# Kernel tuning notes

Hardware: AMD Instinct MI355X
Metric: run time of the kernel (lower is better)

## Reference

```python
import jax, jax.numpy as jnp
import numpy as np

B, N, K, H = 4, 2048, 48, 128
EDGE = 128
FF = 4 * H
SCALE = 30.0


def setup_inputs() -> dict:
    key = jax.random.key(0)
    ks = jax.random.split(key, 12)
    s = lambda fan_in: 1.0 / np.sqrt(fan_in)
    return {
        "h_V": jax.random.normal(ks[0], (B, N, H), jnp.float32),
        "h_E": jax.random.normal(ks[1], (B, N, K, EDGE), jnp.float32),
        "E_idx": jax.random.randint(ks[2], (B, N, K), 0, N, jnp.int32),
        "mask_V": jnp.ones((B, N), jnp.float32),
        "mask_attend": jnp.ones((B, N, K), jnp.float32),
        "W1_w": jax.random.normal(ks[3], (H + EDGE, H), jnp.float32) * s(H + EDGE),
        "W1_b": jnp.zeros((H,), jnp.float32),
        "W2_w": jax.random.normal(ks[4], (H, H), jnp.float32) * s(H),
        "W2_b": jnp.zeros((H,), jnp.float32),
        "W3_w": jax.random.normal(ks[5], (H, H), jnp.float32) * s(H),
        "W3_b": jnp.zeros((H,), jnp.float32),
        "Win_w": jax.random.normal(ks[6], (H, FF), jnp.float32) * s(H),
        "Win_b": jnp.zeros((FF,), jnp.float32),
        "Wout_w": jax.random.normal(ks[7], (FF, H), jnp.float32) * s(FF),
        "Wout_b": jnp.zeros((H,), jnp.float32),
    }


def reference(h_V, h_E, E_idx, mask_V, mask_attend,
              W1_w, W1_b, W2_w, W2_b, W3_w, W3_b,
              Win_w, Win_b, Wout_w, Wout_b):
    gelu_tanh = lambda x: jax.nn.gelu(x, approximate=True)   # self.act = jax.nn.gelu (default approx)
    gelu_exact = lambda x: jax.nn.gelu(x, approximate=False)  # FFN uses approximate=False

    # gather neighbor node features: [B,N,K,H]
    h_nb = jax.vmap(lambda hv, idx: hv[idx])(h_V, E_idx)
    h_EV = jnp.concatenate([h_nb, h_E], axis=-1)              # [B,N,K,H+EDGE]

    # 3-layer message MLP
    m = gelu_tanh(jnp.einsum('bnkc,ch->bnkh', h_EV, W1_w) + W1_b)
    m = gelu_tanh(jnp.einsum('bnkh,hg->bnkg', m, W2_w) + W2_b)
    m = jnp.einsum('bnkg,gh->bnkh', m, W3_w) + W3_b

    m = mask_attend[..., None] * m
    dh = jnp.sum(m, axis=-2) / SCALE                          # [B,N,H]
    h = h_V + dh                                              # dropout rate 0 (eval)

    # position-wise FFN
    ff = gelu_exact(jnp.einsum('bnh,hf->bnf', h, Win_w) + Win_b)
    dh2 = jnp.einsum('bnf,fh->bnh', ff, Wout_w) + Wout_b
    h = h + dh2

    return mask_V[..., None] * h
```

## Files before the change

### kernel.cpp

```cpp
#include <hip/hip_runtime.h>
#include <hip/hip_bf16.h>
#include <math.h>

typedef __attribute__((ext_vector_type(8))) short bf16x8;
typedef __attribute__((ext_vector_type(4))) float f32x4;

#define MFMA16(a,b,c) __builtin_amdgcn_mfma_f32_16x16x32_bf16((a),(b),(c),0,0,0)

__device__ __forceinline__ unsigned int pack2(float a, float b){
  __hip_bfloat162 h = __float22bfloat162_rn(float2{a, b});
  union { __hip_bfloat162 h; unsigned int u; } v; v.h = h;
  return v.u;
}
__device__ __forceinline__ float gelu_tanh_f(float x){
  float x2 = x * x;
  float z  = x * fmaf(x2, -0.10294823f, -2.3022082f);
  float e  = exp2f(z);
  return x * __builtin_amdgcn_rcpf(1.0f + e);
}
__device__ __forceinline__ float gelu_erf_f(float x){
  return 0.5f * x * (1.0f + erff(x * 0.70710678118654752f));
}

__global__ void k_prep(const float* __restrict__ W1, const float* __restrict__ W2,
                       const float* __restrict__ W3, const float* __restrict__ Win,
                       const float* __restrict__ Wout, unsigned short* __restrict__ wt)
{
  int t = blockIdx.x * 256 + threadIdx.x;
  if (t >= 196608) return;
  float v;
  if (t < 32768){            int o = t >> 8,        i = t & 255;         v = W1[i*128 + o]; }
  else if (t < 49152){       int l = t - 32768, o = l >> 7, i = l & 127; v = W2[i*128 + o]; }
  else if (t < 65536){       int l = t - 49152, o = l >> 7, i = l & 127; v = W3[i*128 + o]; }
  else if (t < 131072){      int l = t - 65536, o = l >> 7, i = l & 127; v = Win[i*512 + o]; }
  else {                     int l = t - 131072, o = l >> 9, i = l & 511; v = Wout[i*128 + o]; }
  union { float f; unsigned int u; } w; w.f = v;
  unsigned int r = w.u + 0x7fffu + ((w.u >> 16) & 1u);
  wt[t] = (unsigned short)(r >> 16);
}

__global__ __launch_bounds__(256)
void k_hvp(const float* __restrict__ hV, const unsigned short* __restrict__ wt,
           const float* __restrict__ b1, float* __restrict__ hVp)
{
  __shared__ char sH[32*256];
  const int tid = threadIdx.x;
  const int wv  = tid >> 6;
  const int ln  = tid & 63;
  const int l15 = ln & 15;
  const int l4  = ln >> 4;
  const int swz = (l15 & 7) << 4;
  const unsigned short* W1T = wt;
  const int nb = blockIdx.x * 32;

#pragma unroll
  for (int it = 0; it < 2; ++it){
    int cid = tid + it*256;
    int r = cid >> 4, cb = cid & 15;
    const float* src = hV + (size_t)(nb + r)*128 + cb*8;
    float4 a0 = *(const float4*)(src);
    float4 a1 = *(const float4*)(src + 4);
    uint4 w;
    w.x = pack2(a0.x, a0.y); w.y = pack2(a0.z, a0.w);
    w.z = pack2(a1.x, a1.y); w.w = pack2(a1.z, a1.w);
    *(uint4*)(&sH[r*256 + ((cb*16) ^ ((r&7)<<4))]) = w;
  }
  __syncthreads();

  f32x4 acc[2][2];
#pragma unroll
  for (int m = 0; m < 2; ++m){ acc[m][0] = f32x4{0.f,0.f,0.f,0.f}; acc[m][1] = f32x4{0.f,0.f,0.f,0.f}; }
#pragma unroll
  for (int ks = 0; ks < 4; ++ks){
    bf16x8 x0 = *(const bf16x8*)(&sH[(l15)*256      + ((ks*64 + l4*16) ^ swz)]);
    bf16x8 x1 = *(const bf16x8*)(&sH[(16 + l15)*256 + ((ks*64 + l4*16) ^ swz)]);
#pragma unroll
    for (int m = 0; m < 2; ++m){
      int orow = (wv*2 + m)*16 + l15;
      bf16x8 wf = *(const bf16x8*)(W1T + orow*256 + ks*32 + l4*8);
      acc[m][0] = MFMA16(wf, x0, acc[m][0]);
      acc[m][1] = MFMA16(wf, x1, acc[m][1]);
    }
  }
#pragma unroll
  for (int m = 0; m < 2; ++m){
    int och0 = (wv*2 + m)*16 + l4*4;
    float q0 = b1[och0], q1 = b1[och0+1], q2 = b1[och0+2], q3 = b1[och0+3];
#pragma unroll
    for (int nt = 0; nt < 2; ++nt){
      int node = nb + nt*16 + l15;
      float4 o;
      o.x = acc[m][nt][0] + q0;
      o.y = acc[m][nt][1] + q1;
      o.z = acc[m][nt][2] + q2;
      o.w = acc[m][nt][3] + q3;
      *(float4*)(hVp + (size_t)node*128 + och0) = o;
    }
  }
}

#define NPB 4
__global__ __launch_bounds__(512, 4)
void k_msg(const float* __restrict__ hE, const int* __restrict__ Eidx,
           const float* __restrict__ maskA, const unsigned short* __restrict__ wt,
           const float* __restrict__ hVp, const float* __restrict__ b2,
           float* __restrict__ S, float* __restrict__ msums)
{
  __shared__ char sE0[12288];
  __shared__ char sE1[12288];
  __shared__ char sM [12288];

  const int tid = threadIdx.x;
  const int wv  = tid >> 6;
  const int ln  = tid & 63;
  const int l15 = ln & 15;
  const int l4  = ln >> 4;
  const int swz = (l15 & 7) << 4;

  const unsigned short* W1T = wt;
  const unsigned short* W2T = wt + 32768;

  bf16x8 w1f[4], w2f[4];
  {
    int orow = wv*16 + l15;
#pragma unroll
    for (int ks = 0; ks < 4; ++ks){
      w1f[ks] = *(const bf16x8*)(W1T + orow*256 + 128 + ks*32 + l4*8);
      w2f[ks] = *(const bf16x8*)(W2T + orow*128 + ks*32 + l4*8);
    }
  }
  const int och0 = wv*16 + l4*4;
  const float4 b2q = *(const float4*)(b2 + och0);

  int xoff[4];
#pragma unroll
  for (int ks = 0; ks < 4; ++ks) xoff[ks] = l15*256 + ((ks*64 + l4*16) ^ swz);
  const int woff  = l15*256 + ((och0*2) ^ swz);
  const int soff0 = (tid>>5)*256 + (((tid&31)*8) ^ (((tid>>5)&7)<<4));

  const int node0 = blockIdx.x * NPB;

  float4 e0, e1, e2;
  int pidx0, pidx1, pidx2; float pmk0, pmk1, pmk2;
  {
    const float4* ef = (const float4*)(hE + (size_t)node0 * 6144);
    e0 = ef[tid]; e1 = ef[tid + 512]; e2 = ef[tid + 1024];
    const int* ip = Eidx + node0*48 + l15;
    pidx0 = ip[0]; pidx1 = ip[16]; pidx2 = ip[32];
    const float* mp = maskA + node0*48 + l15;
    pmk0 = mp[0]; pmk1 = mp[16]; pmk2 = mp[32];
  }

  auto body = [&](char* sE, int node){
    const int b = node >> 11;
    const float mk0 = pmk0, mk1 = pmk1, mk2 = pmk2;
    float4 hp0, hp1, hp2;
    {
      const float* base = hVp + ((size_t)(b << 11)) * 128 + och0;
      hp0 = *(const float4*)(base + (size_t)pidx0 * 128);
      hp1 = *(const float4*)(base + (size_t)pidx1 * 128);
      hp2 = *(const float4*)(base + (size_t)pidx2 * 128);
    }
    {
      uint2 p;
      p.x = pack2(e0.x, e0.y); p.y = pack2(e0.z, e0.w);
      *(uint2*)(sE + soff0) = p;
      p.x = pack2(e1.x, e1.y); p.y = pack2(e1.z, e1.w);
      *(uint2*)(sE + soff0 + 4096) = p;
      p.x = pack2(e2.x, e2.y); p.y = pack2(e2.z, e2.w);
      *(uint2*)(sE + soff0 + 8192) = p;
    }
    {
      int pn = (node + 1 < 8192) ? node + 1 : node;
      const float4* ef = (const float4*)(hE + (size_t)pn * 6144);
      e0 = ef[tid]; e1 = ef[tid + 512]; e2 = ef[tid + 1024];
      const int* ip = Eidx + pn*48 + l15;
      pidx0 = ip[0]; pidx1 = ip[16]; pidx2 = ip[32];
      const float* mp = maskA + pn*48 + l15;
      pmk0 = mp[0]; pmk1 = mp[16]; pmk2 = mp[32];
    }
    __syncthreads();

    f32x4 a0 = f32x4{0.f,0.f,0.f,0.f}, a1 = a0, a2 = a0;
#pragma unroll
    for (int ks = 0; ks < 4; ++ks){
      bf16x8 x0 = *(const bf16x8*)(sE + xoff[ks]);
      bf16x8 x1 = *(const bf16x8*)(sE + xoff[ks] + 4096);
      bf16x8 x2 = *(const bf16x8*)(sE + xoff[ks] + 8192);
      a0 = MFMA16(w1f[ks], x0, a0);
      a1 = MFMA16(w1f[ks], x1, a1);
      a2 = MFMA16(w1f[ks], x2, a2);
    }
    {
      uint2 p;
      p.x = pack2(gelu_tanh_f(a0[0] + hp0.x), gelu_tanh_f(a0[1] + hp0.y));
      p.y = pack2(gelu_tanh_f(a0[2] + hp0.z), gelu_tanh_f(a0[3] + hp0.w));
      *(uint2*)(sM + woff) = p;
      p.x = pack2(gelu_tanh_f(a1[0] + hp1.x), gelu_tanh_f(a1[1] + hp1.y));
      p.y = pack2(gelu_tanh_f(a1[2] + hp1.z), gelu_tanh_f(a1[3] + hp1.w));
      *(uint2*)(sM + woff + 4096) = p;
      p.x = pack2(gelu_tanh_f(a2[0] + hp2.x), gelu_tanh_f(a2[1] + hp2.y));
      p.y = pack2(gelu_tanh_f(a2[2] + hp2.z), gelu_tanh_f(a2[3] + hp2.w));
      *(uint2*)(sM + woff + 8192) = p;
    }
    __syncthreads();

    a0 = f32x4{0.f,0.f,0.f,0.f}; a1 = a0; a2 = a0;
#pragma unroll
    for (int ks = 0; ks < 4; ++ks){
      bf16x8 x0 = *(const bf16x8*)(sM + xoff[ks]);
      bf16x8 x1 = *(const bf16x8*)(sM + xoff[ks] + 4096);
      bf16x8 x2 = *(const bf16x8*)(sM + xoff[ks] + 8192);
      a0 = MFMA16(w2f[ks], x0, a0);
      a1 = MFMA16(w2f[ks], x1, a1);
      a2 = MFMA16(w2f[ks], x2, a2);
    }
    {
      float s0, s1, s2, s3;
      s0  = mk0 * gelu_tanh_f(a0[0] + b2q.x);
      s1  = mk0 * gelu_tanh_f(a0[1] + b2q.y);
      s2  = mk0 * gelu_tanh_f(a0[2] + b2q.z);
      s3  = mk0 * gelu_tanh_f(a0[3] + b2q.w);
      s0 += mk1 * gelu_tanh_f(a1[0] + b2q.x);
      s1 += mk1 * gelu_tanh_f(a1[1] + b2q.y);
      s2 += mk1 * gelu_tanh_f(a1[2] + b2q.z);
      s3 += mk1 * gelu_tanh_f(a1[3] + b2q.w);
      s0 += mk2 * gelu_tanh_f(a2[0] + b2q.x);
      s1 += mk2 * gelu_tanh_f(a2[1] + b2q.y);
      s2 += mk2 * gelu_tanh_f(a2[2] + b2q.z);
      s3 += mk2 * gelu_tanh_f(a2[3] + b2q.w);
#pragma unroll
      for (int off = 1; off < 16; off <<= 1){
        s0 += __shfl_xor(s0, off, 16);
        s1 += __shfl_xor(s1, off, 16);
        s2 += __shfl_xor(s2, off, 16);
        s3 += __shfl_xor(s3, off, 16);
      }
      if (l15 == 0){
        float4 o;
        o.x = s0 * (1.0f/30.0f);
        o.y = s1 * (1.0f/30.0f);
        o.z = s2 * (1.0f/30.0f);
        o.w = s3 * (1.0f/30.0f);
        *(float4*)(S + (size_t)node*128 + och0) = o;
      }
      if (wv == 0){
        float q = mk0 + mk1 + mk2;
#pragma unroll
        for (int off = 1; off < 16; off <<= 1) q += __shfl_xor(q, off, 16);
        if (ln == 0) msums[node] = q * (1.0f/30.0f);
      }
    }
  };

#pragma unroll
  for (int i = 0; i < NPB; i += 2){
    body(sE0, node0 + i);
    body(sE1, node0 + i + 1);
  }
}

__global__ __launch_bounds__(256, 2)
void k_ffn(const float* __restrict__ hV, const float* __restrict__ S,
           const float* __restrict__ msums, const float* __restrict__ maskV,
           const unsigned short* __restrict__ wt,
           const float* __restrict__ b3, const float* __restrict__ bin,
           const float* __restrict__ bout, float* __restrict__ out)
{
  __shared__ char  sS[32*256];
  __shared__ char  sH[32*256];
  __shared__ float sHf[32*132];
  __shared__ char  sF[32*1024];

  const int tid = threadIdx.x;
  const int wv  = tid >> 6;
  const int ln  = tid & 63;
  const int l15 = ln & 15;
  const int l4  = ln >> 4;
  const int swz = (l15 & 7) << 4;
  const unsigned short* W3T   = wt + 49152;
  const unsigned short* WinT  = wt + 65536;
  const unsigned short* WoutT = wt + 131072;
  const int nb = blockIdx.x * 32;

#pragma unroll
  for (int it = 0; it < 2; ++it){
    int cid = tid + it*256;
    int r = cid >> 4, cb = cid & 15;
    const float* src = S + (size_t)(nb + r)*128 + cb*8;
    float4 a0 = *(const float4*)(src);
    float4 a1 = *(const float4*)(src + 4);
    uint4 w;
    w.x = pack2(a0.x, a0.y); w.y = pack2(a0.z, a0.w);
    w.z = pack2(a1.x, a1.y); w.w = pack2(a1.z, a1.w);
    *(uint4*)(&sS[r*256 + ((cb*16) ^ ((r&7)<<4))]) = w;
  }
  __syncthreads();

  {
    f32x4 acc[2][2];
#pragma unroll
    for (int m = 0; m < 2; ++m){ acc[m][0] = f32x4{0.f,0.f,0.f,0.f}; acc[m][1] = f32x4{0.f,0.f,0.f,0.f}; }
#pragma unroll
    for (int ks = 0; ks < 4; ++ks){
      bf16x8 x0 = *(const bf16x8*)(&sS[(l15)*256      + ((ks*64 + l4*16) ^ swz)]);
      bf16x8 x1 = *(const bf16x8*)(&sS[(16 + l15)*256 + ((ks*64 + l4*16) ^ swz)]);
#pragma unroll
      for (int m = 0; m < 2; ++m){
        int cr = (wv*2 + m)*16 + l15;
        bf16x8 wf = *(const bf16x8*)(W3T + cr*128 + ks*32 + l4*8);
        acc[m][0] = MFMA16(wf, x0, acc[m][0]);
        acc[m][1] = MFMA16(wf, x1, acc[m][1]);
      }
    }
#pragma unroll
    for (int m = 0; m < 2; ++m){
      int ch0 = (wv*2 + m)*16 + l4*4;
      const float4 b3q = *(const float4*)(b3 + ch0);
#pragma unroll
      for (int nt = 0; nt < 2; ++nt){
        int row  = nt*16 + l15;
        int node = nb + row;
        float ms = msums[node];
        const float4 hv = *(const float4*)(hV + (size_t)node*128 + ch0);
        float h0 = hv.x + acc[m][nt][0] + ms*b3q.x;
        float h1 = hv.y + acc[m][nt][1] + ms*b3q.y;
        float h2 = hv.z + acc[m][nt][2] + ms*b3q.z;
        float h3 = hv.w + acc[m][nt][3] + ms*b3q.w;
        float4 hf; hf.x = h0; hf.y = h1; hf.z = h2; hf.w = h3;
        *(float4*)(&sHf[row*132 + ch0]) = hf;
        uint2 p; p.x = pack2(h0, h1); p.y = pack2(h2, h3);
        *(uint2*)(&sH[row*256 + ((ch0*2) ^ ((row&7)<<4))]) = p;
      }
    }
  }
  __syncthreads();

  f32x4 accA[8][2];
#pragma unroll
  for (int m8 = 0; m8 < 8; ++m8){ accA[m8][0] = f32x4{0.f,0.f,0.f,0.f}; accA[m8][1] = f32x4{0.f,0.f,0.f,0.f}; }
#pragma unroll
  for (int ks = 0; ks < 4; ++ks){
    bf16x8 x0 = *(const bf16x8*)(&sH[(l15)*256      + ((ks*64 + l4*16) ^ swz)]);
    bf16x8 x1 = *(const bf16x8*)(&sH[(16 + l15)*256 + ((ks*64 + l4*16) ^ swz)]);
#pragma unroll
    for (int m8 = 0; m8 < 8; ++m8){
      int fr = (wv*8 + m8)*16 + l15;
      bf16x8 wf = *(const bf16x8*)(WinT + fr*128 + ks*32 + l4*8);
      accA[m8][0] = MFMA16(wf, x0, accA[m8][0]);
      accA[m8][1] = MFMA16(wf, x1, accA[m8][1]);
    }
  }
#pragma unroll
  for (int m8 = 0; m8 < 8; ++m8){
    int f0 = (wv*8 + m8)*16 + l4*4;
    float q0 = bin[f0], q1 = bin[f0+1], q2 = bin[f0+2], q3 = bin[f0+3];
#pragma unroll
    for (int nt = 0; nt < 2; ++nt){
      int row = nt*16 + l15;
      float g0 = gelu_erf_f(accA[m8][nt][0] + q0);
      float g1 = gelu_erf_f(accA[m8][nt][1] + q1);
      float g2 = gelu_erf_f(accA[m8][nt][2] + q2);
      float g3 = gelu_erf_f(accA[m8][nt][3] + q3);
      uint2 p; p.x = pack2(g0, g1); p.y = pack2(g2, g3);
      *(uint2*)(&sF[row*1024 + ((f0*2) ^ swz)]) = p;
    }
  }
  __syncthreads();

  f32x4 accB[2][2];
#pragma unroll
  for (int m = 0; m < 2; ++m){ accB[m][0] = f32x4{0.f,0.f,0.f,0.f}; accB[m][1] = f32x4{0.f,0.f,0.f,0.f}; }
#pragma unroll
  for (int ks = 0; ks < 16; ++ks){
    bf16x8 x0 = *(const bf16x8*)(&sF[(l15)*1024      + ((ks*64 + l4*16) ^ swz)]);
    bf16x8 x1 = *(const bf16x8*)(&sF[(16 + l15)*1024 + ((ks*64 + l4*16) ^ swz)]);
#pragma unroll
    for (int m = 0; m < 2; ++m){
      int cr = (wv*2 + m)*16 + l15;
      bf16x8 wf = *(const bf16x8*)(WoutT + cr*512 + ks*32 + l4*8);
      accB[m][0] = MFMA16(wf, x0, accB[m][0]);
      accB[m][1] = MFMA16(wf, x1, accB[m][1]);
    }
  }
#pragma unroll
  for (int m = 0; m < 2; ++m){
    int ch0 = (wv*2 + m)*16 + l4*4;
    float q0 = bout[ch0], q1 = bout[ch0+1], q2 = bout[ch0+2], q3 = bout[ch0+3];
#pragma unroll
    for (int nt = 0; nt < 2; ++nt){
      int row  = nt*16 + l15;
      int node = nb + row;
      float mv = maskV[node];
      const float4 hf = *(const float4*)(&sHf[row*132 + ch0]);
      float4 o;
      o.x = mv * (hf.x + accB[m][nt][0] + q0);
      o.y = mv * (hf.y + accB[m][nt][1] + q1);
      o.z = mv * (hf.z + accB[m][nt][2] + q2);
      o.w = mv * (hf.w + accB[m][nt][3] + q3);
      *(float4*)(out + (size_t)node*128 + ch0) = o;
    }
  }
}

extern "C" void kernel_launch(void* const* d_in, const int* in_sizes, int n_in,
                              void* d_out, int out_size, void* d_ws, size_t ws_size,
                              hipStream_t stream)
{
  const float* hV    = (const float*)d_in[0];
  const float* hE    = (const float*)d_in[1];
  const int*   Eidx  = (const int*)  d_in[2];
  const float* maskV = (const float*)d_in[3];
  const float* maskA = (const float*)d_in[4];
  const float* W1w = (const float*)d_in[5];
  const float* W1b = (const float*)d_in[6];
  const float* W2w = (const float*)d_in[7];
  const float* W2b = (const float*)d_in[8];
  const float* W3w = (const float*)d_in[9];
  const float* W3b = (const float*)d_in[10];
  const float* Winw  = (const float*)d_in[11];
  const float* Winb  = (const float*)d_in[12];
  const float* Woutw = (const float*)d_in[13];
  const float* Woutb = (const float*)d_in[14];
  float* out = (float*)d_out;

  unsigned short* wt = (unsigned short*)d_ws;
  float* hVp   = (float*)((char*)d_ws + (1u << 19));
  float* Sbuf  = (float*)((char*)d_ws + (1u << 19) + (1u << 22));
  float* msums = (float*)((char*)d_ws + (1u << 19) + (2u << 22));

  k_prep<<<dim3(768),  dim3(256), 0, stream>>>(W1w, W2w, W3w, Winw, Woutw, wt);
  k_hvp <<<dim3(256),  dim3(256), 0, stream>>>(hV, wt, W1b, hVp);
  k_msg <<<dim3(2048), dim3(512), 0, stream>>>(hE, Eidx, maskA, wt, hVp, W2b, Sbuf, msums);
  k_ffn <<<dim3(256),  dim3(256), 0, stream>>>(hV, Sbuf, msums, maskV, wt, W3b, Winb, Woutb, out);
}
```

Baseline: 117.5 us.

## Retile message kernel to two nodes per step and store gathered projections in bf16

The message kernel now handles two nodes per iteration, with two groups of four waves. Each wave computes 32 output channels over 48 edges, so each LDS operand read feeds two MFMAs, and the sE/sM buffers are merged into one double-buffered 24KB buffer. The weight fragments are reloaded from global memory each tile instead of being held in registers, which cuts register pressure but adds L2 traffic. The precomputed h_V projection is stored as bf16, halving the bytes of the random neighbour gather at some precision cost. The grid drops to 1024 blocks, each prefetching the next tile's h_E in bf16-packed registers.

```diff
diff --git a/kernel.cpp b/kernel.cpp
--- a/kernel.cpp
+++ b/kernel.cpp
@@ -12,6 +12,9 @@
   union { __hip_bfloat162 h; unsigned int u; } v; v.h = h;
   return v.u;
 }
+__device__ __forceinline__ float bflo(unsigned int u){ union{unsigned int i; float f;} v; v.i = u << 16; return v.f; }
+__device__ __forceinline__ float bfhi(unsigned int u){ union{unsigned int i; float f;} v; v.i = u & 0xffff0000u; return v.f; }
+
 __device__ __forceinline__ float gelu_tanh_f(float x){
   float x2 = x * x;
   float z  = x * fmaf(x2, -0.10294823f, -2.3022082f);
@@ -41,7 +44,7 @@
 
 __global__ __launch_bounds__(256)
 void k_hvp(const float* __restrict__ hV, const unsigned short* __restrict__ wt,
-           const float* __restrict__ b1, float* __restrict__ hVp)
+           const float* __restrict__ b1, unsigned short* __restrict__ hVpb)
 {
   __shared__ char sH[32*256];
   const int tid = threadIdx.x;
@@ -89,146 +92,177 @@
 #pragma unroll
     for (int nt = 0; nt < 2; ++nt){
       int node = nb + nt*16 + l15;
-      float4 o;
-      o.x = acc[m][nt][0] + q0;
-      o.y = acc[m][nt][1] + q1;
-      o.z = acc[m][nt][2] + q2;
-      o.w = acc[m][nt][3] + q3;
-      *(float4*)(hVp + (size_t)node*128 + och0) = o;
-    }
-  }
-}
-
-#define NPB 4
+      uint2 p;
+      p.x = pack2(acc[m][nt][0] + q0, acc[m][nt][1] + q1);
+      p.y = pack2(acc[m][nt][2] + q2, acc[m][nt][3] + q3);
+      *(uint2*)(hVpb + (size_t)node*128 + och0) = p;
+    }
+  }
+}
+
+#define TPB 4
 __global__ __launch_bounds__(512, 4)
 void k_msg(const float* __restrict__ hE, const int* __restrict__ Eidx,
            const float* __restrict__ maskA, const unsigned short* __restrict__ wt,
-           const float* __restrict__ hVp, const float* __restrict__ b2,
+           const unsigned short* __restrict__ hVpb, const float* __restrict__ b2,
            float* __restrict__ S, float* __restrict__ msums)
 {
-  __shared__ char sE0[12288];
-  __shared__ char sE1[12288];
-  __shared__ char sM [12288];
+  __shared__ char sB0[24576];
+  __shared__ char sB1[24576];
 
   const int tid = threadIdx.x;
   const int wv  = tid >> 6;
   const int ln  = tid & 63;
   const int l15 = ln & 15;
   const int l4  = ln >> 4;
+  const int g   = wv >> 2;
+  const int cw  = wv & 3;
   const int swz = (l15 & 7) << 4;
 
   const unsigned short* W1T = wt;
   const unsigned short* W2T = wt + 32768;
 
-  bf16x8 w1f[4], w2f[4];
+  const int chm0 = cw*32 + l4*4;
+  const float4 b2q0 = *(const float4*)(b2 + chm0);
+  const float4 b2q1 = *(const float4*)(b2 + chm0 + 16);
+
+  int xoff[4];
+#pragma unroll
+  for (int ks = 0; ks < 4; ++ks) xoff[ks] = (g*48 + l15)*256 + ((ks*64 + l4*16) ^ swz);
+  const int woff0 = (g*48 + l15)*256 + (((cw*64)      + l4*8) ^ swz);
+  const int woff1 = (g*48 + l15)*256 + (((cw*64 + 32) + l4*8) ^ swz);
+  const int soff0 = (tid>>5)*256 + (((tid&31)*8) ^ (((tid>>5)&7)<<4));
+
+  const int tile0 = blockIdx.x * TPB;
+
+  uint2 pe[6]; int nidx[3]; float nmk[3];
   {
-    int orow = wv*16 + l15;
+    const float4* ef = (const float4*)(hE + (size_t)tile0 * 12288);
+#pragma unroll
+    for (int j = 0; j < 6; ++j){
+      float4 v = ef[tid + j*512];
+      pe[j].x = pack2(v.x, v.y); pe[j].y = pack2(v.z, v.w);
+    }
+    const int n0 = tile0*2 + g;
+    const int*   ip = Eidx  + n0*48 + l15;
+    const float* mp = maskA + n0*48 + l15;
+#pragma unroll
+    for (int q = 0; q < 3; ++q){ nidx[q] = ip[q*16]; nmk[q] = mp[q*16]; }
+  }
+
+  for (int t = 0; t < TPB; ++t){
+    char* sB = (t & 1) ? sB1 : sB0;
+    const int n = (tile0 + t)*2 + g;
+    const size_t bb = ((size_t)(n >> 11)) << 11;
+
+    const int   ci0 = nidx[0], ci1 = nidx[1], ci2 = nidx[2];
+    const float mk0 = nmk[0],  mk1 = nmk[1],  mk2 = nmk[2];
+
+#pragma unroll
+    for (int j = 0; j < 6; ++j) *(uint2*)(sB + soff0 + j*4096) = pe[j];
+
+    if (t + 1 < TPB){
+      const float4* ef = (const float4*)(hE + (size_t)(tile0 + t + 1) * 12288);
+#pragma unroll
+      for (int j = 0; j < 6; ++j){
+        float4 v = ef[tid + j*512];
+        pe[j].x = pack2(v.x, v.y); pe[j].y = pack2(v.z, v.w);
+      }
+      const int nn = (tile0 + t + 1)*2 + g;
+      const int*   ip = Eidx  + nn*48 + l15;
+      const float* mp = maskA + nn*48 + l15;
+#pragma unroll
+      for (int q = 0; q < 3; ++q){ nidx[q] = ip[q*16]; nmk[q] = mp[q*16]; }
+    }
+
+    bf16x8 w1f[2][4];
+#pragma unroll
+    for (int m = 0; m < 2; ++m)
+#pragma unroll
+      for (int ks = 0; ks < 4; ++ks)
+        w1f[m][ks] = *(const bf16x8*)(W1T + (cw*32 + m*16 + l15)*256 + 128 + ks*32 + l4*8);
+
+    __syncthreads();
+
+    uint2 hp[2][3];
+#pragma unroll
+    for (int m = 0; m < 2; ++m){
+      hp[m][0] = *(const uint2*)(hVpb + (bb + (size_t)ci0)*128 + chm0 + m*16);
+      hp[m][1] = *(const uint2*)(hVpb + (bb + (size_t)ci1)*128 + chm0 + m*16);
+      hp[m][2] = *(const uint2*)(hVpb + (bb + (size_t)ci2)*128 + chm0 + m*16);
+    }
+
+    f32x4 acc[2][3];
+#pragma unroll
+    for (int m = 0; m < 2; ++m)
+#pragma unroll
+      for (int q = 0; q < 3; ++q) acc[m][q] = f32x4{0.f,0.f,0.f,0.f};
 #pragma unroll
     for (int ks = 0; ks < 4; ++ks){
-      w1f[ks] = *(const bf16x8*)(W1T + orow*256 + 128 + ks*32 + l4*8);
-      w2f[ks] = *(const bf16x8*)(W2T + orow*128 + ks*32 + l4*8);
-    }
-  }
-  const int och0 = wv*16 + l4*4;
-  const float4 b2q = *(const float4*)(b2 + och0);
-
-  int xoff[4];
-#pragma unroll
-  for (int ks = 0; ks < 4; ++ks) xoff[ks] = l15*256 + ((ks*64 + l4*16) ^ swz);
-  const int woff  = l15*256 + ((och0*2) ^ swz);
-  const int soff0 = (tid>>5)*256 + (((tid&31)*8) ^ (((tid>>5)&7)<<4));
-
-  const int node0 = blockIdx.x * NPB;
-
-  float4 e0, e1, e2;
-  int pidx0, pidx1, pidx2; float pmk0, pmk1, pmk2;
-  {
-    const float4* ef = (const float4*)(hE + (size_t)node0 * 6144);
-    e0 = ef[tid]; e1 = ef[tid + 512]; e2 = ef[tid + 1024];
-    const int* ip = Eidx + node0*48 + l15;
-    pidx0 = ip[0]; pidx1 = ip[16]; pidx2 = ip[32];
-    const float* mp = maskA + node0*48 + l15;
-    pmk0 = mp[0]; pmk1 = mp[16]; pmk2 = mp[32];
-  }
-
-  auto body = [&](char* sE, int node){
-    const int b = node >> 11;
-    const float mk0 = pmk0, mk1 = pmk1, mk2 = pmk2;
-    float4 hp0, hp1, hp2;
-    {
-      const float* base = hVp + ((size_t)(b << 11)) * 128 + och0;
-      hp0 = *(const float4*)(base + (size_t)pidx0 * 128);
-      hp1 = *(const float4*)(base + (size_t)pidx1 * 128);
-      hp2 = *(const float4*)(base + (size_t)pidx2 * 128);
-    }
-    {
-      uint2 p;
-      p.x = pack2(e0.x, e0.y); p.y = pack2(e0.z, e0.w);
-      *(uint2*)(sE + soff0) = p;
-      p.x = pack2(e1.x, e1.y); p.y = pack2(e1.z, e1.w);
-      *(uint2*)(sE + soff0 + 4096) = p;
-      p.x = pack2(e2.x, e2.y); p.y = pack2(e2.z, e2.w);
-      *(uint2*)(sE + soff0 + 8192) = p;
-    }
-    {
-      int pn = (node + 1 < 8192) ? node + 1 : node;
-      const float4* ef = (const float4*)(hE + (size_t)pn * 6144);
-      e0 = ef[tid]; e1 = ef[tid + 512]; e2 = ef[tid + 1024];
-      const int* ip = Eidx + pn*48 + l15;
-      pidx0 = ip[0]; pidx1 = ip[16]; pidx2 = ip[32];
-      const float* mp = maskA + pn*48 + l15;
-      pmk0 = mp[0]; pmk1 = mp[16]; pmk2 = mp[32];
-    }
+#pragma unroll
+      for (int q = 0; q < 3; ++q){
+        bf16x8 x = *(const bf16x8*)(sB + xoff[ks] + q*4096);
+        acc[0][q] = MFMA16(w1f[0][ks], x, acc[0][q]);
+        acc[1][q] = MFMA16(w1f[1][ks], x, acc[1][q]);
+      }
+    }
+
     __syncthreads();
 
-    f32x4 a0 = f32x4{0.f,0.f,0.f,0.f}, a1 = a0, a2 = a0;
+#pragma unroll
+    for (int m = 0; m < 2; ++m){
+      const int wo = m ? woff1 : woff0;
+#pragma unroll
+      for (int q = 0; q < 3; ++q){
+        uint2 h = hp[m][q];
+        uint2 p;
+        p.x = pack2(gelu_tanh_f(acc[m][q][0] + bflo(h.x)),
+                    gelu_tanh_f(acc[m][q][1] + bfhi(h.x)));
+        p.y = pack2(gelu_tanh_f(acc[m][q][2] + bflo(h.y)),
+                    gelu_tanh_f(acc[m][q][3] + bfhi(h.y)));
+        *(uint2*)(sB + wo + q*4096) = p;
+      }
+    }
+
+    bf16x8 w2f[2][4];
+#pragma unroll
+    for (int m = 0; m < 2; ++m)
+#pragma unroll
+      for (int ks = 0; ks < 4; ++ks)
+        w2f[m][ks] = *(const bf16x8*)(W2T + (cw*32 + m*16 + l15)*128 + ks*32 + l4*8);
+
+    __syncthreads();
+
+#pragma unroll
+    for (int m = 0; m < 2; ++m)
+#pragma unroll
+      for (int q = 0; q < 3; ++q) acc[m][q] = f32x4{0.f,0.f,0.f,0.f};
 #pragma unroll
     for (int ks = 0; ks < 4; ++ks){
-      bf16x8 x0 = *(const bf16x8*)(sE + xoff[ks]);
-      bf16x8 x1 = *(const bf16x8*)(sE + xoff[ks] + 4096);
-      bf16x8 x2 = *(const bf16x8*)(sE + xoff[ks] + 8192);
-      a0 = MFMA16(w1f[ks], x0, a0);
-      a1 = MFMA16(w1f[ks], x1, a1);
-      a2 = MFMA16(w1f[ks], x2, a2);
-    }
-    {
-      uint2 p;
-      p.x = pack2(gelu_tanh_f(a0[0] + hp0.x), gelu_tanh_f(a0[1] + hp0.y));
-      p.y = pack2(gelu_tanh_f(a0[2] + hp0.z), gelu_tanh_f(a0[3] + hp0.w));
-      *(uint2*)(sM + woff) = p;
-      p.x = pack2(gelu_tanh_f(a1[0] + hp1.x), gelu_tanh_f(a1[1] + hp1.y));
-      p.y = pack2(gelu_tanh_f(a1[2] + hp1.z), gelu_tanh_f(a1[3] + hp1.w));
-      *(uint2*)(sM + woff + 4096) = p;
-      p.x = pack2(gelu_tanh_f(a2[0] + hp2.x), gelu_tanh_f(a2[1] + hp2.y));
-      p.y = pack2(gelu_tanh_f(a2[2] + hp2.z), gelu_tanh_f(a2[3] + hp2.w));
-      *(uint2*)(sM + woff + 8192) = p;
-    }
-    __syncthreads();
-
-    a0 = f32x4{0.f,0.f,0.f,0.f}; a1 = a0; a2 = a0;
-#pragma unroll
-    for (int ks = 0; ks < 4; ++ks){
-      bf16x8 x0 = *(const bf16x8*)(sM + xoff[ks]);
-      bf16x8 x1 = *(const bf16x8*)(sM + xoff[ks] + 4096);
-      bf16x8 x2 = *(const bf16x8*)(sM + xoff[ks] + 8192);
-      a0 = MFMA16(w2f[ks], x0, a0);
-      a1 = MFMA16(w2f[ks], x1, a1);
-      a2 = MFMA16(w2f[ks], x2, a2);
-    }
-    {
+#pragma unroll
+      for (int q = 0; q < 3; ++q){
+        bf16x8 x = *(const bf16x8*)(sB + xoff[ks] + q*4096);
+        acc[0][q] = MFMA16(w2f[0][ks], x, acc[0][q]);
+        acc[1][q] = MFMA16(w2f[1][ks], x, acc[1][q]);
+      }
+    }
+
+#pragma unroll
+    for (int m = 0; m < 2; ++m){
+      const float4 bq = m ? b2q1 : b2q0;
       float s0, s1, s2, s3;
-      s0  = mk0 * gelu_tanh_f(a0[0] + b2q.x);
-      s1  = mk0 * gelu_tanh_f(a0[1] + b2q.y);
-      s2  = mk0 * gelu_tanh_f(a0[2] + b2q.z);
-      s3  = mk0 * gelu_tanh_f(a0[3] + b2q.w);
-      s0 += mk1 * gelu_tanh_f(a1[0] + b2q.x);
-      s1 += mk1 * gelu_tanh_f(a1[1] + b2q.y);
-      s2 += mk1 * gelu_tanh_f(a1[2] + b2q.z);
-      s3 += mk1 * gelu_tanh_f(a1[3] + b2q.w);
-      s0 += mk2 * gelu_tanh_f(a2[0] + b2q.x);
-      s1 += mk2 * gelu_tanh_f(a2[1] + b2q.y);
-      s2 += mk2 * gelu_tanh_f(a2[2] + b2q.z);
-      s3 += mk2 * gelu_tanh_f(a2[3] + b2q.w);
+      s0  = mk0 * gelu_tanh_f(acc[m][0][0] + bq.x);
+      s1  = mk0 * gelu_tanh_f(acc[m][0][1] + bq.y);
+      s2  = mk0 * gelu_tanh_f(acc[m][0][2] + bq.z);
+      s3  = mk0 * gelu_tanh_f(acc[m][0][3] + bq.w);
+      s0 += mk1 * gelu_tanh_f(acc[m][1][0] + bq.x);
+      s1 += mk1 * gelu_tanh_f(acc[m][1][1] + bq.y);
+      s2 += mk1 * gelu_tanh_f(acc[m][1][2] + bq.z);
+      s3 += mk1 * gelu_tanh_f(acc[m][1][3] + bq.w);
+      s0 += mk2 * gelu_tanh_f(acc[m][2][0] + bq.x);
+      s1 += mk2 * gelu_tanh_f(acc[m][2][1] + bq.y);
+      s2 += mk2 * gelu_tanh_f(acc[m][2][2] + bq.z);
+      s3 += mk2 * gelu_tanh_f(acc[m][2][3] + bq.w);
 #pragma unroll
       for (int off = 1; off < 16; off <<= 1){
         s0 += __shfl_xor(s0, off, 16);
@@ -242,21 +276,15 @@
         o.y = s1 * (1.0f/30.0f);
         o.z = s2 * (1.0f/30.0f);
         o.w = s3 * (1.0f/30.0f);
-        *(float4*)(S + (size_t)node*128 + och0) = o;
-      }
-      if (wv == 0){
-        float q = mk0 + mk1 + mk2;
-#pragma unroll
-        for (int off = 1; off < 16; off <<= 1) q += __shfl_xor(q, off, 16);
-        if (ln == 0) msums[node] = q * (1.0f/30.0f);
-      }
-    }
-  };
-
-#pragma unroll
-  for (int i = 0; i < NPB; i += 2){
-    body(sE0, node0 + i);
-    body(sE1, node0 + i + 1);
+        *(float4*)(S + (size_t)n*128 + chm0 + m*16) = o;
+      }
+    }
+    if (cw == 0){
+      float qsum = mk0 + mk1 + mk2;
+#pragma unroll
+      for (int off = 1; off < 16; off <<= 1) qsum += __shfl_xor(qsum, off, 16);
+      if (ln == 0) msums[n] = qsum * (1.0f/30.0f);
+    }
   }
 }
 
@@ -424,13 +452,13 @@
   const float* Woutb = (const float*)d_in[14];
   float* out = (float*)d_out;
 
-  unsigned short* wt = (unsigned short*)d_ws;
-  float* hVp   = (float*)((char*)d_ws + (1u << 19));
-  float* Sbuf  = (float*)((char*)d_ws + (1u << 19) + (1u << 22));
-  float* msums = (float*)((char*)d_ws + (1u << 19) + (2u << 22));
+  unsigned short* wt   = (unsigned short*)d_ws;
+  unsigned short* hVpb = (unsigned short*)((char*)d_ws + (1u << 19));
+  float* Sbuf  = (float*)((char*)d_ws + (1u << 19) + (1u << 21));
+  float* msums = (float*)((char*)d_ws + (1u << 19) + (1u << 21) + (1u << 22));
 
   k_prep<<<dim3(768),  dim3(256), 0, stream>>>(W1w, W2w, W3w, Winw, Woutw, wt);
-  k_hvp <<<dim3(256),  dim3(256), 0, stream>>>(hV, wt, W1b, hVp);
-  k_msg <<<dim3(2048), dim3(512), 0, stream>>>(hE, Eidx, maskA, wt, hVp, W2b, Sbuf, msums);
+  k_hvp <<<dim3(256),  dim3(256), 0, stream>>>(hV, wt, W1b, hVpb);
+  k_msg <<<dim3(1024), dim3(512), 0, stream>>>(hE, Eidx, maskA, wt, hVpb, W2b, Sbuf, msums);
   k_ffn <<<dim3(256),  dim3(256), 0, stream>>>(hV, Sbuf, msums, maskV, wt, W3b, Winb, Woutb, out);
 }
```

Result: slower. 213.4 us (+81.6%).
